# Kernel tuning notes

Hardware: AMD Instinct MI355X
Metric: run time of the kernel (lower is better)

The kernel has to match this reference:

```python
import jax, jax.numpy as jnp
import numpy as np

B, S, D, H = 2, 4096, 768, 12
DH = D // H
SCALE = 1.0 / DH ** 0.5


def setup_inputs() -> dict:
    key = jax.random.key(0)
    k1, k2, k3, k4, k5 = jax.random.split(key, 5)
    x = jax.random.normal(k1, (B, S, D), dtype=jnp.float32)
    # nn.Linear weights: stored as [out, in]; init ~ U(-1/sqrt(in), 1/sqrt(in))
    lim = 1.0 / np.sqrt(D)
    W_qkv = jax.random.uniform(k2, (3 * D, D), minval=-lim, maxval=lim, dtype=jnp.float32)
    b_qkv = jax.random.uniform(k3, (3 * D,), minval=-lim, maxval=lim, dtype=jnp.float32)
    W_out = jax.random.uniform(k4, (D, D), minval=-lim, maxval=lim, dtype=jnp.float32)
    b_out = jax.random.uniform(k5, (D,), minval=-lim, maxval=lim, dtype=jnp.float32)
    return {"x": x, "W_qkv": W_qkv, "b_qkv": b_qkv, "W_out": W_out, "b_out": b_out}


def reference(x, W_qkv, b_qkv, W_out, b_out):
    bs, ns, _ = x.shape
    qkv = x @ W_qkv.T + b_qkv                       # [B, S, 3D]
    qkv = qkv.reshape(bs, ns, 3, H, DH)
    qkv = jnp.transpose(qkv, (2, 0, 3, 1, 4))        # [3, B, H, S, DH]
    q, k, v = qkv[0], qkv[1], qkv[2]
    attn = jnp.einsum('bhqd,bhkd->bhqk', q, k)       # [B, H, S, S]
    attn = jax.nn.softmax(attn * SCALE, axis=-1)
    out = jnp.einsum('bhqk,bhkd->bhqd', attn, v)     # [B, H, S, DH]
    out = jnp.transpose(out, (0, 2, 1, 3)).reshape(bs, ns, D)
    return out @ W_out.T + b_out
```

## Files before the change

kernel.cpp:

```cpp
#include <hip/hip_runtime.h>
#include <hip/hip_bf16.h>
#include <stdint.h>

#define B_    2
#define S_    4096
#define D_    768
#define H_    12
#define DH_   64
#define BH_   (B_*H_)
#define M_    (B_*S_)
#define NQKV_ 2304
#define QSCALE_ 0.18033688011112042f

typedef unsigned short bf16u;
typedef short bf16x8 __attribute__((ext_vector_type(8)));
typedef float f32x4 __attribute__((ext_vector_type(4)));

__device__ __forceinline__ bf16u f2bf(float f) {
    unsigned u = __float_as_uint(f);
    u += 0x7FFFu + ((u >> 16) & 1u);
    return (bf16u)(u >> 16);
}

__device__ __forceinline__ void gl_lds16(const void* g, void* l) {
    __builtin_amdgcn_global_load_lds(
        (const __attribute__((address_space(1))) unsigned*)g,
        (__attribute__((address_space(3))) unsigned*)l, 16, 0, 0);
}

__global__ __launch_bounds__(256) void convert_kernel(
    const float* __restrict__ src, bf16u* __restrict__ dst, int n4)
{
    int i = blockIdx.x * 256 + threadIdx.x;
    if (i < n4) {
        float4 v = ((const float4*)src)[i];
        ushort4 o;
        o.x = f2bf(v.x); o.y = f2bf(v.y); o.z = f2bf(v.z); o.w = f2bf(v.w);
        ((ushort4*)dst)[i] = o;
    }
}

template<int EPI>
__global__ __launch_bounds__(256) void gemm_kernel(
    const bf16u* __restrict__ A, const bf16u* __restrict__ Bw,
    const float* __restrict__ bias, float* __restrict__ Cout,
    bf16u* __restrict__ Qb, bf16u* __restrict__ Kb, bf16u* __restrict__ Vtb)
{
    __shared__ bf16u As[128*32];
    __shared__ bf16u Bs[128*32];
    const int tid  = threadIdx.x;
    const int lane = tid & 63;
    const int wave = tid >> 6;
    const int wr = wave >> 1, wc = wave & 1;
    const int lr = lane & 15;
    const int quad = lane >> 4;
    const int m0 = blockIdx.y * 128;
    const int n0 = blockIdx.x * 128;

    f32x4 acc[4][4];
    #pragma unroll
    for (int i = 0; i < 4; i++)
        #pragma unroll
        for (int j = 0; j < 4; j++)
            acc[i][j] = (f32x4){0.f, 0.f, 0.f, 0.f};

    for (int k0 = 0; k0 < 768; k0 += 32) {
        #pragma unroll
        for (int r = 0; r < 2; r++) {
            int c = r * 256 + tid;
            int row = c >> 2;
            int col = ((c & 3) ^ (row & 3)) * 8;
            gl_lds16(A  + (size_t)(m0 + row) * 768 + k0 + col, (char*)As + c * 16);
            gl_lds16(Bw + (size_t)(n0 + row) * 768 + k0 + col, (char*)Bs + c * 16);
        }
        __syncthreads();
        bf16x8 af[4], bg[4];
        #pragma unroll
        for (int t = 0; t < 4; t++) {
            int ra = wr * 64 + t * 16 + lr;
            int rb = wc * 64 + t * 16 + lr;
            af[t] = *(const bf16x8*)(As + ra * 32 + ((quad ^ (ra & 3)) * 8));
            bg[t] = *(const bf16x8*)(Bs + rb * 32 + ((quad ^ (rb & 3)) * 8));
        }
        #pragma unroll
        for (int i = 0; i < 4; i++)
            #pragma unroll
            for (int j = 0; j < 4; j++)
                acc[i][j] = __builtin_amdgcn_mfma_f32_16x16x32_bf16(
                    af[i], bg[j], acc[i][j], 0, 0, 0);
        __syncthreads();
    }

    #pragma unroll
    for (int i = 0; i < 4; i++) {
        int mbase = m0 + wr * 64 + i * 16 + quad * 4;
        #pragma unroll
        for (int j = 0; j < 4; j++) {
            int n = n0 + wc * 64 + j * 16 + lr;
            float bv = bias[n];
            if (EPI == 0) {
                #pragma unroll
                for (int r = 0; r < 4; r++)
                    Cout[(size_t)(mbase + r) * 768 + n] = acc[i][j][r] + bv;
            } else {
                int t3  = n / 768;
                int rem = n - t3 * 768;
                int h   = rem >> 6;
                int dh  = rem & 63;
                #pragma unroll
                for (int r = 0; r < 4; r++) {
                    int mm = mbase + r;
                    int b  = mm >> 12;
                    int s  = mm & 4095;
                    int bh = b * H_ + h;
                    float v = acc[i][j][r] + bv;
                    if (t3 == 0)
                        Qb[((size_t)bh * S_ + s) * DH_ + dh] = f2bf(v * QSCALE_);
                    else if (t3 == 1)
                        Kb[((size_t)bh * S_ + s) * DH_ + dh] = f2bf(v);
                    else
                        Vtb[((size_t)bh * DH_ + dh) * S_ + s] = f2bf(v);
                }
            }
        }
    }
}

#define PS_STRIDE 72

__global__ __launch_bounds__(256, 3) void attn_kernel(
    const bf16u* __restrict__ Qb, const bf16u* __restrict__ Kb,
    const bf16u* __restrict__ Vtb, bf16u* __restrict__ A2)
{
    __shared__ bf16u Ks[2][64*64];
    __shared__ bf16u Vs[2][64*64];
    __shared__ bf16u Ps[4][32*PS_STRIDE];
    const int tid  = threadIdx.x;
    const int lane = tid & 63;
    const int w    = tid >> 6;
    const int lr   = lane & 15;
    const int quad = lane >> 4;
    const int q0   = blockIdx.x * 128;
    const int bh   = blockIdx.y;

    const size_t kbase_g = (size_t)bh * S_ * DH_;
    const size_t vbase_g = (size_t)bh * DH_ * S_;

    bf16x8 aq[2][2];
    #pragma unroll
    for (int rh = 0; rh < 2; rh++) {
        const size_t qb = ((size_t)bh * S_ + q0 + w * 32 + rh * 16 + lr) * DH_ + quad * 8;
        aq[rh][0] = *(const bf16x8*)(Qb + qb);
        aq[rh][1] = *(const bf16x8*)(Qb + qb + 32);
    }

    bf16x8 onesf;
    #pragma unroll
    for (int j = 0; j < 8; j++) onesf[j] = (short)0x3F80;

    f32x4 o[2][4];
    f32x4 l_acc[2];
    #pragma unroll
    for (int rh = 0; rh < 2; rh++) {
        l_acc[rh] = (f32x4){0.f, 0.f, 0.f, 0.f};
        #pragma unroll
        for (int t = 0; t < 4; t++)
            o[rh][t] = (f32x4){0.f, 0.f, 0.f, 0.f};
    }

    int kvoff[4][2];
    #pragma unroll
    for (int nt = 0; nt < 4; nt++) {
        int rk = nt * 16 + lr;
        kvoff[nt][0] = rk * 64 + ((quad ^ (rk & 7)) * 8);
        kvoff[nt][1] = rk * 64 + (((4 + quad) ^ (rk & 7)) * 8);
    }
    bf16u* pw[2];
    #pragma unroll
    for (int rh = 0; rh < 2; rh++)
        pw[rh] = &Ps[w][(rh * 16 + lr) * PS_STRIDE];

    auto stage = [&](int kv0, int bf) {
        #pragma unroll
        for (int r = 0; r < 2; r++) {
            int c = r * 256 + tid;
            int row = c >> 3;
            int col = ((c & 7) ^ (row & 7)) * 8;
            gl_lds16(Kb  + kbase_g + (size_t)(kv0 + row) * DH_ + col,
                     (char*)&Ks[bf][0] + c * 16);
            gl_lds16(Vtb + vbase_g + (size_t)row * S_ + kv0 + col,
                     (char*)&Vs[bf][0] + c * 16);
        }
    };

    stage(0, 0);

    auto body = [&](int it, int buf, bool do_stage) __attribute__((always_inline)) {
        __syncthreads();
        if (do_stage) stage((it + 1) * 64, buf ^ 1);

        const bf16u* Kbuf = &Ks[buf][0];
        const bf16u* Vbuf = &Vs[buf][0];

        f32x4 sc[2][4];
        __builtin_amdgcn_s_setprio(1);
        #pragma unroll
        for (int nt = 0; nt < 4; nt++) {
            const bf16x8 bk0 = *(const bf16x8*)(Kbuf + kvoff[nt][0]);
            const bf16x8 bk1 = *(const bf16x8*)(Kbuf + kvoff[nt][1]);
            #pragma unroll
            for (int rh = 0; rh < 2; rh++) {
                f32x4 s = (f32x4){0.f, 0.f, 0.f, 0.f};
                s = __builtin_amdgcn_mfma_f32_16x16x32_bf16(bk0, aq[rh][0], s, 0, 0, 0);
                s = __builtin_amdgcn_mfma_f32_16x16x32_bf16(bk1, aq[rh][1], s, 0, 0, 0);
                sc[rh][nt] = s;
            }
        }
        __builtin_amdgcn_s_setprio(0);

        #pragma unroll
        for (int rh = 0; rh < 2; rh++) {
            #pragma unroll
            for (int nt = 0; nt < 4; nt++) {
                float p0 = __builtin_amdgcn_exp2f(sc[rh][nt][0]);
                float p1 = __builtin_amdgcn_exp2f(sc[rh][nt][1]);
                float p2 = __builtin_amdgcn_exp2f(sc[rh][nt][2]);
                float p3 = __builtin_amdgcn_exp2f(sc[rh][nt][3]);
                unsigned w0 = __builtin_amdgcn_perm(__float_as_uint(p1),
                                                    __float_as_uint(p0), 0x07060302u);
                unsigned w1 = __builtin_amdgcn_perm(__float_as_uint(p3),
                                                    __float_as_uint(p2), 0x07060302u);
                *(uint2*)(pw[rh] + nt * 16 + quad * 4) = make_uint2(w0, w1);
            }
        }

        __asm__ volatile("s_waitcnt lgkmcnt(0)" ::: "memory");

        __builtin_amdgcn_s_setprio(1);
        #pragma unroll
        for (int rh = 0; rh < 2; rh++) {
            const bf16x8 ap0 = *(const bf16x8*)(pw[rh] + quad * 8);
            const bf16x8 ap1 = *(const bf16x8*)(pw[rh] + 32 + quad * 8);
            l_acc[rh] = __builtin_amdgcn_mfma_f32_16x16x32_bf16(ap0, onesf, l_acc[rh], 0, 0, 0);
            l_acc[rh] = __builtin_amdgcn_mfma_f32_16x16x32_bf16(ap1, onesf, l_acc[rh], 0, 0, 0);
            #pragma unroll
            for (int nt = 0; nt < 4; nt++) {
                const bf16x8 bv0 = *(const bf16x8*)(Vbuf + kvoff[nt][0]);
                const bf16x8 bv1 = *(const bf16x8*)(Vbuf + kvoff[nt][1]);
                o[rh][nt] = __builtin_amdgcn_mfma_f32_16x16x32_bf16(ap0, bv0, o[rh][nt], 0, 0, 0);
                o[rh][nt] = __builtin_amdgcn_mfma_f32_16x16x32_bf16(ap1, bv1, o[rh][nt], 0, 0, 0);
            }
        }
        __builtin_amdgcn_s_setprio(0);
    };

    #pragma unroll 1
    for (int it = 0; it < S_ / 64 - 2; it += 2) {
        body(it,     0, true);
        body(it + 1, 1, true);
    }
    body(S_ / 64 - 2, 0, true);
    body(S_ / 64 - 1, 1, false);

    const int b = bh / H_, h = bh % H_;
    #pragma unroll
    for (int rh = 0; rh < 2; rh++) {
        float rl[4];
        #pragma unroll
        for (int r2 = 0; r2 < 4; r2++) rl[r2] = 1.0f / l_acc[rh][r2];
        #pragma unroll
        for (int nt = 0; nt < 4; nt++)
            #pragma unroll
            for (int r2 = 0; r2 < 4; r2++) {
                int q = q0 + w * 32 + rh * 16 + quad * 4 + r2;
                float v = o[rh][nt][r2] * rl[r2];
                A2[((size_t)b * S_ + q) * D_ + h * DH_ + nt * 16 + lr] = f2bf(v);
            }
    }
}

extern "C" void kernel_launch(void* const* d_in, const int* in_sizes, int n_in,
                              void* d_out, int out_size, void* d_ws, size_t ws_size,
                              hipStream_t stream) {
    const float* x     = (const float*)d_in[0];
    const float* W_qkv = (const float*)d_in[1];
    const float* b_qkv = (const float*)d_in[2];
    const float* W_out = (const float*)d_in[3];
    const float* b_out = (const float*)d_in[4];
    float* out = (float*)d_out;
    char* ws = (char*)d_ws;

    bf16u* xb    = (bf16u*)(ws + 0);
    bf16u* wqkvb = (bf16u*)(ws + 12582912);
    bf16u* woutb = (bf16u*)(ws + 16121856);
    bf16u* Qb    = (bf16u*)(ws + 17301504);
    bf16u* Kb    = (bf16u*)(ws + 29884416);
    bf16u* Vtb   = (bf16u*)(ws + 42467328);
    bf16u* A2    = (bf16u*)(ws + 55050240);

    convert_kernel<<<6291456/4/256, 256, 0, stream>>>(x, xb, 6291456/4);
    convert_kernel<<<1769472/4/256, 256, 0, stream>>>(W_qkv, wqkvb, 1769472/4);
    convert_kernel<<< 589824/4/256, 256, 0, stream>>>(W_out, woutb, 589824/4);

    dim3 g1(NQKV_/128, M_/128);
    gemm_kernel<1><<<g1, 256, 0, stream>>>(xb, wqkvb, b_qkv, nullptr, Qb, Kb, Vtb);

    dim3 g2(S_/128, BH_);
    attn_kernel<<<g2, 256, 0, stream>>>(Qb, Kb, Vtb, A2);

    dim3 g3(D_/128, M_/128);
    gemm_kernel<0><<<g3, 256, 0, stream>>>(A2, woutb, b_out, out, nullptr, nullptr, nullptr);
}
```

Before: 282.8 us.

## Fuse conversions, remap blocks for XCD locality, keep P in registers via permlane swaps

```diff
diff --git a/kernel.cpp b/kernel.cpp
--- a/kernel.cpp
+++ b/kernel.cpp
@@ -28,16 +28,23 @@
         (__attribute__((address_space(3))) unsigned*)l, 16, 0, 0);
 }
 
-__global__ __launch_bounds__(256) void convert_kernel(
-    const float* __restrict__ src, bf16u* __restrict__ dst, int n4)
+#define N1Q_ 1572864
+#define N2Q_  442368
+#define N3Q_  147456
+__global__ __launch_bounds__(256) void convert3_kernel(
+    const float* __restrict__ s1, const float* __restrict__ s2,
+    const float* __restrict__ s3, bf16u* __restrict__ d1,
+    bf16u* __restrict__ d2, bf16u* __restrict__ d3)
 {
     int i = blockIdx.x * 256 + threadIdx.x;
-    if (i < n4) {
-        float4 v = ((const float4*)src)[i];
-        ushort4 o;
-        o.x = f2bf(v.x); o.y = f2bf(v.y); o.z = f2bf(v.z); o.w = f2bf(v.w);
-        ((ushort4*)dst)[i] = o;
-    }
+    const float* s; bf16u* d; int j;
+    if (i < N1Q_)              { s = s1; d = d1; j = i; }
+    else if (i < N1Q_ + N2Q_)  { s = s2; d = d2; j = i - N1Q_; }
+    else                       { s = s3; d = d3; j = i - N1Q_ - N2Q_; }
+    float4 v = ((const float4*)s)[j];
+    ushort4 o;
+    o.x = f2bf(v.x); o.y = f2bf(v.y); o.z = f2bf(v.z); o.w = f2bf(v.w);
+    ((ushort4*)d)[j] = o;
 }
 
 template<int EPI>
@@ -54,8 +61,12 @@
     const int wr = wave >> 1, wc = wave & 1;
     const int lr = lane & 15;
     const int quad = lane >> 4;
-    const int m0 = blockIdx.y * 128;
-    const int n0 = blockIdx.x * 128;
+
+    const int nwg  = gridDim.x * gridDim.y;
+    const int fblk = blockIdx.y * gridDim.x + blockIdx.x;
+    const int vblk = (fblk & 7) * (nwg >> 3) + (fblk >> 3);
+    const int m0 = (vblk / gridDim.x) * 128;
+    const int n0 = (vblk % gridDim.x) * 128;
 
     f32x4 acc[4][4];
     #pragma unroll
@@ -126,22 +137,21 @@
     }
 }
 
-#define PS_STRIDE 72
-
-__global__ __launch_bounds__(256, 3) void attn_kernel(
+__global__ __launch_bounds__(256, 4) void attn_kernel(
     const bf16u* __restrict__ Qb, const bf16u* __restrict__ Kb,
     const bf16u* __restrict__ Vtb, bf16u* __restrict__ A2)
 {
-    __shared__ bf16u Ks[2][64*64];
-    __shared__ bf16u Vs[2][64*64];
-    __shared__ bf16u Ps[4][32*PS_STRIDE];
+    __shared__ char Lds[32768];
     const int tid  = threadIdx.x;
     const int lane = tid & 63;
     const int w    = tid >> 6;
     const int lr   = lane & 15;
     const int quad = lane >> 4;
-    const int q0   = blockIdx.x * 128;
-    const int bh   = blockIdx.y;
+
+    const int fblk = blockIdx.y * gridDim.x + blockIdx.x;
+    const int vblk = (fblk & 7) * 96 + (fblk >> 3);
+    const int q0   = (vblk & 31) * 128;
+    const int bh   = vblk >> 5;
 
     const size_t kbase_g = (size_t)bh * S_ * DH_;
     const size_t vbase_g = (size_t)bh * DH_ * S_;
@@ -164,21 +174,16 @@
     for (int rh = 0; rh < 2; rh++) {
         l_acc[rh] = (f32x4){0.f, 0.f, 0.f, 0.f};
         #pragma unroll
-        for (int t = 0; t < 4; t++)
-            o[rh][t] = (f32x4){0.f, 0.f, 0.f, 0.f};
-    }
-
-    int kvoff[4][2];
+        for (int t = 0; t < 4; t++) o[rh][t] = (f32x4){0.f, 0.f, 0.f, 0.f};
+    }
+
+    int kvaddr[4][2];
     #pragma unroll
     for (int nt = 0; nt < 4; nt++) {
         int rk = nt * 16 + lr;
-        kvoff[nt][0] = rk * 64 + ((quad ^ (rk & 7)) * 8);
-        kvoff[nt][1] = rk * 64 + (((4 + quad) ^ (rk & 7)) * 8);
-    }
-    bf16u* pw[2];
-    #pragma unroll
-    for (int rh = 0; rh < 2; rh++)
-        pw[rh] = &Ps[w][(rh * 16 + lr) * PS_STRIDE];
+        kvaddr[nt][0] = (rk * 64 + ((quad ^ (rk & 7)) * 8)) * 2;
+        kvaddr[nt][1] = (rk * 64 + (((4 + quad) ^ (rk & 7)) * 8)) * 2;
+    }
 
     auto stage = [&](int kv0, int bf) {
         #pragma unroll
@@ -187,9 +192,9 @@
             int row = c >> 3;
             int col = ((c & 7) ^ (row & 7)) * 8;
             gl_lds16(Kb  + kbase_g + (size_t)(kv0 + row) * DH_ + col,
-                     (char*)&Ks[bf][0] + c * 16);
+                     Lds + bf * 8192 + c * 16);
             gl_lds16(Vtb + vbase_g + (size_t)row * S_ + kv0 + col,
-                     (char*)&Vs[bf][0] + c * 16);
+                     Lds + 16384 + bf * 8192 + c * 16);
         }
     };
 
@@ -199,15 +204,15 @@
         __syncthreads();
         if (do_stage) stage((it + 1) * 64, buf ^ 1);
 
-        const bf16u* Kbuf = &Ks[buf][0];
-        const bf16u* Vbuf = &Vs[buf][0];
+        const char* Kbuf = Lds + buf * 8192;
+        const char* Vbuf = Lds + 16384 + buf * 8192;
 
         f32x4 sc[2][4];
         __builtin_amdgcn_s_setprio(1);
         #pragma unroll
         for (int nt = 0; nt < 4; nt++) {
-            const bf16x8 bk0 = *(const bf16x8*)(Kbuf + kvoff[nt][0]);
-            const bf16x8 bk1 = *(const bf16x8*)(Kbuf + kvoff[nt][1]);
+            const bf16x8 bk0 = *(const bf16x8*)(Kbuf + kvaddr[nt][0]);
+            const bf16x8 bk1 = *(const bf16x8*)(Kbuf + kvaddr[nt][1]);
             #pragma unroll
             for (int rh = 0; rh < 2; rh++) {
                 f32x4 s = (f32x4){0.f, 0.f, 0.f, 0.f};
@@ -218,6 +223,7 @@
         }
         __builtin_amdgcn_s_setprio(0);
 
+        unsigned W[2][4][2];
         #pragma unroll
         for (int rh = 0; rh < 2; rh++) {
             #pragma unroll
@@ -226,29 +232,46 @@
                 float p1 = __builtin_amdgcn_exp2f(sc[rh][nt][1]);
                 float p2 = __builtin_amdgcn_exp2f(sc[rh][nt][2]);
                 float p3 = __builtin_amdgcn_exp2f(sc[rh][nt][3]);
-                unsigned w0 = __builtin_amdgcn_perm(__float_as_uint(p1),
-                                                    __float_as_uint(p0), 0x07060302u);
-                unsigned w1 = __builtin_amdgcn_perm(__float_as_uint(p3),
-                                                    __float_as_uint(p2), 0x07060302u);
-                *(uint2*)(pw[rh] + nt * 16 + quad * 4) = make_uint2(w0, w1);
-            }
-        }
-
-        __asm__ volatile("s_waitcnt lgkmcnt(0)" ::: "memory");
+                W[rh][nt][0] = __builtin_amdgcn_perm(__float_as_uint(p1),
+                                                     __float_as_uint(p0), 0x07060302u);
+                W[rh][nt][1] = __builtin_amdgcn_perm(__float_as_uint(p3),
+                                                     __float_as_uint(p2), 0x07060302u);
+            }
+        }
+
+        bf16x8 ap[2][2];
+        #pragma unroll
+        for (int rh = 0; rh < 2; rh++) {
+            #pragma unroll
+            for (int ks = 0; ks < 2; ks++) {
+                union { unsigned u[4]; bf16x8 v; } Af;
+                #pragma unroll
+                for (int b = 0; b < 2; b++) {
+                    auto r1 = __builtin_amdgcn_permlane32_swap(
+                        W[rh][2 * ks][b], W[rh][2 * ks + 1][b], false, false);
+                    auto r2 = __builtin_amdgcn_permlane16_swap(
+                        r1[0], r1[1], false, false);
+                    Af.u[b]     = r2[0];
+                    Af.u[2 + b] = r2[1];
+                }
+                ap[rh][ks] = Af.v;
+            }
+        }
 
         __builtin_amdgcn_s_setprio(1);
         #pragma unroll
         for (int rh = 0; rh < 2; rh++) {
-            const bf16x8 ap0 = *(const bf16x8*)(pw[rh] + quad * 8);
-            const bf16x8 ap1 = *(const bf16x8*)(pw[rh] + 32 + quad * 8);
-            l_acc[rh] = __builtin_amdgcn_mfma_f32_16x16x32_bf16(ap0, onesf, l_acc[rh], 0, 0, 0);
-            l_acc[rh] = __builtin_amdgcn_mfma_f32_16x16x32_bf16(ap1, onesf, l_acc[rh], 0, 0, 0);
-            #pragma unroll
-            for (int nt = 0; nt < 4; nt++) {
-                const bf16x8 bv0 = *(const bf16x8*)(Vbuf + kvoff[nt][0]);
-                const bf16x8 bv1 = *(const bf16x8*)(Vbuf + kvoff[nt][1]);
-                o[rh][nt] = __builtin_amdgcn_mfma_f32_16x16x32_bf16(ap0, bv0, o[rh][nt], 0, 0, 0);
-                o[rh][nt] = __builtin_amdgcn_mfma_f32_16x16x32_bf16(ap1, bv1, o[rh][nt], 0, 0, 0);
+            l_acc[rh] = __builtin_amdgcn_mfma_f32_16x16x32_bf16(ap[rh][0], onesf, l_acc[rh], 0, 0, 0);
+            l_acc[rh] = __builtin_amdgcn_mfma_f32_16x16x32_bf16(ap[rh][1], onesf, l_acc[rh], 0, 0, 0);
+        }
+        #pragma unroll
+        for (int nt = 0; nt < 4; nt++) {
+            const bf16x8 bv0 = *(const bf16x8*)(Vbuf + kvaddr[nt][0]);
+            const bf16x8 bv1 = *(const bf16x8*)(Vbuf + kvaddr[nt][1]);
+            #pragma unroll
+            for (int rh = 0; rh < 2; rh++) {
+                o[rh][nt] = __builtin_amdgcn_mfma_f32_16x16x32_bf16(ap[rh][0], bv0, o[rh][nt], 0, 0, 0);
+                o[rh][nt] = __builtin_amdgcn_mfma_f32_16x16x32_bf16(ap[rh][1], bv1, o[rh][nt], 0, 0, 0);
             }
         }
         __builtin_amdgcn_s_setprio(0);
@@ -298,9 +321,8 @@
     bf16u* Vtb   = (bf16u*)(ws + 42467328);
     bf16u* A2    = (bf16u*)(ws + 55050240);
 
-    convert_kernel<<<6291456/4/256, 256, 0, stream>>>(x, xb, 6291456/4);
-    convert_kernel<<<1769472/4/256, 256, 0, stream>>>(W_qkv, wqkvb, 1769472/4);
-    convert_kernel<<< 589824/4/256, 256, 0, stream>>>(W_out, woutb, 589824/4);
+    convert3_kernel<<<(N1Q_ + N2Q_ + N3Q_) / 256, 256, 0, stream>>>(
+        x, W_qkv, W_out, xb, wqkvb, woutb);
 
     dim3 g1(NQKV_/128, M_/128);
     gemm_kernel<1><<<g1, 256, 0, stream>>>(xb, wqkvb, b_qkv, nullptr, Qb, Kb, Vtb);
```

Result: no change. 282.0 us (-0.3%).
